# Optimization experiments

Measured on AMD Instinct MI355X. Metric: run time of the kernel, lower is better.

Reference implementation:

```python
import jax, jax.numpy as jnp
import numpy as np

NF, NC = 100000, 10000      # fact / company node counts
EF = 800000                 # edges per relation
DF, DC, H = 768, 128, 128   # fact dim, company dim, hidden
B = 256                     # graphs per batch


def setup_inputs() -> dict:
    key = jax.random.key(0)
    ks = jax.random.split(key, 24)
    s = 0.02
    inp = {
        "x_fact": jax.random.normal(ks[0], (NF, DF), jnp.float32),
        "x_company": jax.random.normal(ks[1], (NC, DC), jnp.float32),
        "ea_fc": jax.random.uniform(ks[2], (EF, 2), jnp.float32),
        "ea_cf": jax.random.uniform(ks[3], (EF, 2), jnp.float32),
        "fc_src": jax.random.randint(ks[4], (EF,), 0, NF),
        "fc_dst": jax.random.randint(ks[5], (EF,), 0, NC),
        "cf_src": jax.random.randint(ks[6], (EF,), 0, NC),
        "cf_dst": jax.random.randint(ks[7], (EF,), 0, NF),
        "batch_fact": jnp.sort(jax.random.randint(ks[8], (NF,), 0, B)),
        # edge gate Linear(2,1)
        "Wm": jax.random.normal(ks[9], (2, 1), jnp.float32) * s,
        "bm": jnp.zeros((1,), jnp.float32),
        # layer 1 GCNConv weights (lin applied to src features)
        "W1_fc": jax.random.normal(ks[10], (DF, H), jnp.float32) * s,
        "b1_fc": jnp.zeros((H,), jnp.float32),
        "W1_cf": jax.random.normal(ks[11], (DC, H), jnp.float32) * s,
        "b1_cf": jnp.zeros((H,), jnp.float32),
        # layer 2
        "W2_fc": jax.random.normal(ks[12], (H, H), jnp.float32) * s,
        "b2_fc": jnp.zeros((H,), jnp.float32),
        "W2_cf": jax.random.normal(ks[13], (H, H), jnp.float32) * s,
        "b2_cf": jnp.zeros((H,), jnp.float32),
        # classifier Linear(H, 1)
        "Wc": jax.random.normal(ks[14], (H, 1), jnp.float32) * s,
        "bc": jnp.zeros((1,), jnp.float32),
    }
    return inp


def _inv_sqrt(d):
    return jnp.where(d > 0, jax.lax.rsqrt(d), 0.0)


def _gcn(x_src, W, b, src, dst, w, n_src, n_dst):
    # symmetric-normalized weighted GCN conv (bipartite, no self loops)
    deg_s = jax.ops.segment_sum(w, src, num_segments=n_src)
    deg_d = jax.ops.segment_sum(w, dst, num_segments=n_dst)
    norm = w * _inv_sqrt(deg_s)[src] * _inv_sqrt(deg_d)[dst]  # [E]
    h = x_src @ W                                             # [n_src, H]
    out = jax.ops.segment_sum(norm[:, None] * h[src], dst, num_segments=n_dst)
    return out + b


def reference(x_fact, x_company, ea_fc, ea_cf, fc_src, fc_dst, cf_src, cf_dst,
              batch_fact, Wm, bm, W1_fc, b1_fc, W1_cf, b1_cf,
              W2_fc, b2_fc, W2_cf, b2_cf, Wc, bc):
    # learned per-edge gate: [sentiment, decay] -> sigmoid -> [0,1]
    w_fc = jax.nn.sigmoid(ea_fc @ Wm + bm)[:, 0]
    w_cf = jax.nn.sigmoid(ea_cf @ Wm + bm)[:, 0]

    # layer 1 (HeteroConv, aggr='sum'; one relation per dst type)
    c1 = jax.nn.relu(_gcn(x_fact, W1_fc, b1_fc, fc_src, fc_dst, w_fc, NF, NC))
    f1 = jax.nn.relu(_gcn(x_company, W1_cf, b1_cf, cf_src, cf_dst, w_cf, NC, NF))

    # layer 2
    c2 = jax.nn.relu(_gcn(f1, W2_fc, b2_fc, fc_src, fc_dst, w_fc, NF, NC))
    f2 = jax.nn.relu(_gcn(c1, W2_cf, b2_cf, cf_src, cf_dst, w_cf, NC, NF))

    # readout='fact': global mean pool over fact nodes per graph
    sums = jax.ops.segment_sum(f2, batch_fact, num_segments=B)        # [B, H]
    cnts = jax.ops.segment_sum(jnp.ones((NF,), f2.dtype), batch_fact, num_segments=B)
    pooled = sums / jnp.maximum(cnts, 1.0)[:, None]

    return (pooled @ Wc + bc)[:, 0]  # [B] logits
```

## Files before the change

kernel.cpp:

```cpp
#include <hip/hip_runtime.h>
#include <hip/hip_bf16.h>

#define NF 100000
#define NC 10000
#define EF 800000
#define DF 768
#define DC 128
#define H  128
#define B  256

#define GB1 782
#define GATEB 6250
#define SFC 192
#define SCF 32
#define MASK40 0xFFFFFFFFFFULL
#define FIXSCALE 1073741824.0f
#define INVFIX (1.0f/1073741824.0f)

typedef __bf16 bf16x8 __attribute__((ext_vector_type(8)));
typedef float  f32x4  __attribute__((ext_vector_type(4)));

#define GLD_LDS16(g, l) \
    __builtin_amdgcn_global_load_lds((const __attribute__((address_space(1))) void*)(g), \
                                     (__attribute__((address_space(3))) void*)(l), 16, 0, 0)

__global__ __launch_bounds__(256) void init_kernel(float4* __restrict__ zp, int nz4, int zb,
                                                   const float* __restrict__ W1,
                                                   __bf16* __restrict__ b1h,
                                                   __bf16* __restrict__ b1l) {
    if ((int)blockIdx.x < zb) {
        int i = blockIdx.x * 256 + threadIdx.x;
        if (i < nz4) zp[i] = make_float4(0.f, 0.f, 0.f, 0.f);
        return;
    }
    int idx = ((int)blockIdx.x - zb) * 256 + threadIdx.x;
    if (idx < DF * H) {
        int k = idx >> 7, n = idx & 127;
        float x = W1[idx];
        __bf16 h = (__bf16)x;
        b1h[n * DF + k] = h;
        b1l[n * DF + k] = (__bf16)(x - (float)h);
    }
}

__global__ __launch_bounds__(256) void gemm1_gate_kernel(
        const float* __restrict__ A,
        const __bf16* __restrict__ Bth, const __bf16* __restrict__ Btl,
        __bf16* __restrict__ Cb,
        const float* __restrict__ ea_fc, const float* __restrict__ ea_cf,
        const int* __restrict__ fc_src, const int* __restrict__ fc_dst,
        const int* __restrict__ cf_src, const int* __restrict__ cf_dst,
        const float* __restrict__ Wm, const float* __restrict__ bm,
        float* __restrict__ deg_s_fc, float* __restrict__ deg_s_cf,
        unsigned long long* __restrict__ packed_all,
        float2* __restrict__ pack_fc, float2* __restrict__ pack_cf) {
    __shared__ __attribute__((aligned(16))) __bf16 Bs[2][8192];
    const int K = DF, M = NF;
    int t = threadIdx.x;

    if ((int)blockIdx.x < GB1) {
        int lane = t & 63, wave = t >> 6;
        int row0 = blockIdx.x * 128;
        int m0 = wave * 32;
        int mrow = lane & 15;
        int kq = (lane >> 4) * 8;

        int soff[4];
        #pragma unroll
        for (int i = 0; i < 4; i++) {
            int s = wave * 256 + i * 64 + lane;
            int ks = s >> 9, nt = (s >> 6) & 7;
            int n  = nt * 16 + (lane & 15);
            int kk = ks * 32 + (lane >> 4) * 8;
            soff[i] = n * K + kk;
        }

        f32x4 acc[2][8] = {};

        for (int k0 = 0; k0 < K; k0 += 64) {
            __syncthreads();
            #pragma unroll
            for (int i = 0; i < 4; i++) {
                int base = (wave * 256 + i * 64) * 8;
                GLD_LDS16(Bth + soff[i] + k0, &Bs[0][base]);
                GLD_LDS16(Btl + soff[i] + k0, &Bs[1][base]);
            }
            bf16x8 ah[2][2], al[2][2];
            #pragma unroll
            for (int mt = 0; mt < 2; mt++) {
                int gr = row0 + m0 + mt * 16 + mrow;
                #pragma unroll
                for (int ks = 0; ks < 2; ks++) {
                    float f[8] = {0.f,0.f,0.f,0.f,0.f,0.f,0.f,0.f};
                    if (gr < M) {
                        const float* ap = &A[(size_t)gr * K + k0 + ks * 32 + kq];
                        float4 v0 = *(const float4*)ap;
                        float4 v1 = *(const float4*)(ap + 4);
                        f[0]=v0.x; f[1]=v0.y; f[2]=v0.z; f[3]=v0.w;
                        f[4]=v1.x; f[5]=v1.y; f[6]=v1.z; f[7]=v1.w;
                    }
                    #pragma unroll
                    for (int j = 0; j < 8; j++) {
                        __bf16 h = (__bf16)f[j];
                        ah[mt][ks][j] = h;
                        al[mt][ks][j] = (__bf16)(f[j] - (float)h);
                    }
                }
            }
            __syncthreads();
            #pragma unroll
            for (int ks = 0; ks < 2; ks++) {
                #pragma unroll
                for (int nt = 0; nt < 8; nt++) {
                    int slot = ks * 512 + nt * 64 + lane;
                    bf16x8 bh = *(const bf16x8*)&Bs[0][slot * 8];
                    bf16x8 bl = *(const bf16x8*)&Bs[1][slot * 8];
                    #pragma unroll
                    for (int mt = 0; mt < 2; mt++) {
                        acc[mt][nt] = __builtin_amdgcn_mfma_f32_16x16x32_bf16(ah[mt][ks], bh, acc[mt][nt], 0, 0, 0);
                        acc[mt][nt] = __builtin_amdgcn_mfma_f32_16x16x32_bf16(al[mt][ks], bh, acc[mt][nt], 0, 0, 0);
                        acc[mt][nt] = __builtin_amdgcn_mfma_f32_16x16x32_bf16(ah[mt][ks], bl, acc[mt][nt], 0, 0, 0);
                    }
                }
            }
        }
        #pragma unroll
        for (int mt = 0; mt < 2; mt++) {
            int gr0 = row0 + m0 + mt * 16 + (lane >> 4) * 4;
            #pragma unroll
            for (int nt = 0; nt < 8; nt++) {
                int col = nt * 16 + (lane & 15);
                #pragma unroll
                for (int r = 0; r < 4; r++) {
                    int gr = gr0 + r;
                    if (gr < M) Cb[(size_t)gr * 128 + col] = (__bf16)acc[mt][nt][r];
                }
            }
        }
    } else {
        int e = ((int)blockIdx.x - GB1) * 256 + t;
        bool is_cf = e >= EF;
        int ee = is_cf ? e - EF : e;
        const float2* ea = is_cf ? (const float2*)ea_cf : (const float2*)ea_fc;
        const int* src = is_cf ? cf_src : fc_src;
        const int* dst = is_cf ? cf_dst : fc_dst;
        float2 a = ea[ee];
        float z = a.x * Wm[0] + a.y * Wm[1] + bm[0];
        float w = 1.0f / (1.0f + expf(-z));
        int s = src[ee];
        int d = dst[ee];
        atomicAdd(is_cf ? &deg_s_cf[s] : &deg_s_fc[s], w);
        unsigned long long add = (1ULL << 40) | (unsigned long long)(w * FIXSCALE);
        unsigned long long old = atomicAdd(&packed_all[is_cf ? NC + d : d], add);
        int rank = (int)(old >> 40);
        if (is_cf) {
            if (rank < SCF) pack_cf[(size_t)d * SCF + rank] = make_float2(__int_as_float(s), w);
        } else {
            if (rank < SFC) pack_fc[(size_t)d * SFC + rank] = make_float2(__int_as_float(s), w);
        }
    }
}

__global__ __launch_bounds__(128) void agg_fc_w2_kernel(
        const float2* __restrict__ pack_fc,
        const unsigned long long* __restrict__ packed_fc,
        const float* __restrict__ deg_s_fc,
        const __bf16* __restrict__ h1b,
        const float* __restrict__ b1,
        const float* __restrict__ W2,
        __bf16* __restrict__ h2b) {
    int d = blockIdx.x;
    int t = threadIdx.x;
    unsigned long long pk = packed_fc[d];
    int cnt = (int)(pk >> 40); if (cnt > SFC) cnt = SFC;
    float dd = (float)(pk & MASK40) * INVFIX;
    float rdd = dd > 0.f ? rsqrtf(dd) : 0.f;
    __shared__ float2 s_e[SFC];
    __shared__ float c1row[H];
    const float2* bin = pack_fc + (size_t)d * SFC;
    for (int c = t; c < cnt; c += 128) {
        float2 p = bin[c];
        int s = __float_as_int(p.x);
        s_e[c] = make_float2(p.x, p.y * rsqrtf(deg_s_fc[s]));
    }
    __syncthreads();
    float acc = 0.f;
    #pragma unroll 8
    for (int j = 0; j < cnt; j++) {
        float2 p = s_e[j];
        acc += p.y * (float)h1b[(size_t)__float_as_int(p.x) * H + t];
    }
    float c1v = fmaxf(acc * rdd + b1[t], 0.f);
    c1row[t] = c1v;
    __syncthreads();
    float h2 = 0.f;
    #pragma unroll 8
    for (int k = 0; k < H; k++) h2 += c1row[k] * W2[k * H + t];
    h2b[(size_t)d * H + t] = (__bf16)h2;
}

#define FPB 8
__global__ __launch_bounds__(128) void agg_cf_pool_kernel(
        const float2* __restrict__ pack_cf,
        const unsigned long long* __restrict__ packed_cf,
        const float* __restrict__ deg_s_cf,
        const __bf16* __restrict__ h2b,
        const float* __restrict__ b2,
        const int* __restrict__ batch,
        float* __restrict__ pooled,
        float* __restrict__ bcnt) {
    int t = threadIdx.x;
    int f0 = blockIdx.x * FPB;
    __shared__ float2 s_e[FPB * SCF];
    __shared__ int   s_cnt[FPB];
    __shared__ int   s_batch[FPB];
    __shared__ float s_rdd[FPB];
    if (t < FPB) {
        unsigned long long pk = packed_cf[f0 + t];
        int cn = (int)(pk >> 40); if (cn > SCF) cn = SCF;
        s_cnt[t] = cn;
        float dd = (float)(pk & MASK40) * INVFIX;
        s_rdd[t] = dd > 0.f ? rsqrtf(dd) : 0.f;
        s_batch[t] = batch[f0 + t];
    }
    __syncthreads();
    #pragma unroll
    for (int c = 0; c < 2; c++) {
        int sl = c * 128 + t;
        int fl = sl >> 5, r = sl & 31;
        float2 v = make_float2(0.f, 0.f);
        if (r < s_cnt[fl]) {
            float2 p = pack_cf[(size_t)f0 * SCF + sl];
            int s = __float_as_int(p.x);
            v = make_float2(p.x, p.y * rsqrtf(deg_s_cf[s]));
        }
        s_e[sl] = v;
    }
    __syncthreads();
    float acc[FPB];
    #pragma unroll
    for (int f = 0; f < FPB; f++) {
        float a = 0.f;
        int cn = s_cnt[f];
        #pragma unroll 4
        for (int j = 0; j < cn; j++) {
            float2 p = s_e[f * SCF + j];
            a += p.y * (float)h2b[(size_t)__float_as_int(p.x) * H + t];
        }
        acc[f] = a;
    }
    float bval = b2[t];
    int cur_b = -1;
    float accp = 0.f;
    int runc = 0;
    #pragma unroll
    for (int f = 0; f < FPB; f++) {
        float val = fmaxf(acc[f] * s_rdd[f] + bval, 0.f);
        int b = s_batch[f];
        if (b != cur_b) {
            if (cur_b >= 0) {
                atomicAdd(&pooled[cur_b * H + t], accp);
                if (t == 0) atomicAdd(&bcnt[cur_b], (float)runc);
            }
            cur_b = b; accp = 0.f; runc = 0;
        }
        accp += val;
        runc++;
    }
    if (cur_b >= 0) {
        atomicAdd(&pooled[cur_b * H + t], accp);
        if (t == 0) atomicAdd(&bcnt[cur_b], (float)runc);
    }
}

__global__ void final_kernel(const float* __restrict__ pooled,
                             const float* __restrict__ bcnt,
                             const float* __restrict__ Wc,
                             const float* __restrict__ bc,
                             float* __restrict__ out) {
    int b = threadIdx.x;
    float sum = 0.f;
    #pragma unroll 8
    for (int k = 0; k < H; k++) sum += pooled[b * H + k] * Wc[k];
    float c = bcnt[b]; if (c < 1.f) c = 1.f;
    out[b] = sum / c + bc[0];
}

extern "C" void kernel_launch(void* const* d_in, const int* in_sizes, int n_in,
                              void* d_out, int out_size, void* d_ws, size_t ws_size,
                              hipStream_t stream) {
    const float* x_fact = (const float*)d_in[0];
    const float* ea_fc  = (const float*)d_in[2];
    const float* ea_cf  = (const float*)d_in[3];
    const int*   fc_src = (const int*)d_in[4];
    const int*   fc_dst = (const int*)d_in[5];
    const int*   cf_src = (const int*)d_in[6];
    const int*   cf_dst = (const int*)d_in[7];
    const int*   batch  = (const int*)d_in[8];
    const float* Wm     = (const float*)d_in[9];
    const float* bm     = (const float*)d_in[10];
    const float* W1_fc  = (const float*)d_in[11];
    const float* b1_fc  = (const float*)d_in[12];
    const float* W2_cf  = (const float*)d_in[17];
    const float* b2_cf  = (const float*)d_in[18];
    const float* Wc     = (const float*)d_in[19];
    const float* bc     = (const float*)d_in[20];
    float* out = (float*)d_out;

    char* wsb = (char*)d_ws;
    size_t o = 0;
    auto take = [&](size_t bytes) -> char* {
        char* p = wsb + o;
        o += (bytes + 255) & ~(size_t)255;
        return p;
    };

    const size_t PK_B  = ((size_t)(NC + NF) * 8 + 255) & ~(size_t)255;
    const size_t DSF_B = ((size_t)NF * 4 + 255) & ~(size_t)255;
    const size_t DSC_B = ((size_t)NC * 4 + 255) & ~(size_t)255;
    const size_t PL_B  = ((size_t)B * H * 4 + 255) & ~(size_t)255;
    const size_t BC_B  = ((size_t)B * 4 + 255) & ~(size_t)255;
    const size_t ZBYTES = PK_B + DSF_B + DSC_B + PL_B + BC_B;
    char* zbase = take(ZBYTES);
    unsigned long long* packed_all = (unsigned long long*)zbase;
    float* deg_s_fc = (float*)(zbase + PK_B);
    float* deg_s_cf = (float*)(zbase + PK_B + DSF_B);
    float* pooled   = (float*)(zbase + PK_B + DSF_B + DSC_B);
    float* bcnt     = (float*)(zbase + PK_B + DSF_B + DSC_B + PL_B);

    float2* pack_fc = (float2*)take((size_t)NC * SFC * 8);
    float2* pack_cf = (float2*)take((size_t)NF * SCF * 8);
    __bf16* h1b     = (__bf16*)take((size_t)NF * H * 2);
    __bf16* h2b     = (__bf16*)take((size_t)NC * H * 2);
    __bf16* b1h     = (__bf16*)take((size_t)DF * H * 2);
    __bf16* b1l     = (__bf16*)take((size_t)DF * H * 2);

    int nz4 = (int)(ZBYTES / 16);
    int zb = (nz4 + 255) / 256;
    int pb = (DF * H) / 256;
    init_kernel<<<zb + pb, 256, 0, stream>>>((float4*)zbase, nz4, zb, W1_fc, b1h, b1l);

    gemm1_gate_kernel<<<GB1 + GATEB, 256, 0, stream>>>(
        x_fact, b1h, b1l, h1b,
        ea_fc, ea_cf, fc_src, fc_dst, cf_src, cf_dst, Wm, bm,
        deg_s_fc, deg_s_cf, packed_all, pack_fc, pack_cf);

    agg_fc_w2_kernel<<<NC, 128, 0, stream>>>(pack_fc, packed_all, deg_s_fc,
                                             h1b, b1_fc, W2_cf, h2b);

    agg_cf_pool_kernel<<<NF / FPB, 128, 0, stream>>>(pack_cf, packed_all + NC,
                                                     deg_s_cf, h2b, b2_cf,
                                                     batch, pooled, bcnt);

    final_kernel<<<1, 256, 0, stream>>>(pooled, bcnt, Wc, bc, out);
}
```

Baseline: 741.0 us.

## Pad atomic counters, store fp32 features, vectorize gathers, batch gate edges per thread

Pads the per-node packed counters and degree accumulators to stride 8 or 16 elements so atomics on different nodes fall in separate cache lines. Stores h1 and h2 as fp32 instead of bf16 and gathers them with float4 loads, with four thread groups splitting edges and reducing through shared memory. The gate path handles four edges per thread with fewer blocks, and the pooling kernel processes 16 fact nodes per block. The padding greatly enlarges the zeroed region and fp32 features double the gather bytes, which may outweigh the reduced atomic contention.

```diff
diff --git a/kernel.cpp b/kernel.cpp
--- a/kernel.cpp
+++ b/kernel.cpp
@@ -10,9 +10,12 @@
 #define B  256
 
 #define GB1 782
-#define GATEB 6250
+#define GATEB 1563
 #define SFC 192
 #define SCF 32
+#define FPB 16
+#define PKS 8
+#define DSS 16
 #define MASK40 0xFFFFFFFFFFULL
 #define FIXSCALE 1073741824.0f
 #define INVFIX (1.0f/1073741824.0f)
@@ -46,7 +49,7 @@
 __global__ __launch_bounds__(256) void gemm1_gate_kernel(
         const float* __restrict__ A,
         const __bf16* __restrict__ Bth, const __bf16* __restrict__ Btl,
-        __bf16* __restrict__ Cb,
+        float* __restrict__ h1f,
         const float* __restrict__ ea_fc, const float* __restrict__ ea_cf,
         const int* __restrict__ fc_src, const int* __restrict__ fc_dst,
         const int* __restrict__ cf_src, const int* __restrict__ cf_dst,
@@ -133,129 +136,141 @@
                 #pragma unroll
                 for (int r = 0; r < 4; r++) {
                     int gr = gr0 + r;
-                    if (gr < M) Cb[(size_t)gr * 128 + col] = (__bf16)acc[mt][nt][r];
+                    if (gr < M) h1f[(size_t)gr * H + col] = acc[mt][nt][r];
                 }
             }
         }
     } else {
-        int e = ((int)blockIdx.x - GB1) * 256 + t;
-        bool is_cf = e >= EF;
-        int ee = is_cf ? e - EF : e;
-        const float2* ea = is_cf ? (const float2*)ea_cf : (const float2*)ea_fc;
-        const int* src = is_cf ? cf_src : fc_src;
-        const int* dst = is_cf ? cf_dst : fc_dst;
-        float2 a = ea[ee];
-        float z = a.x * Wm[0] + a.y * Wm[1] + bm[0];
-        float w = 1.0f / (1.0f + expf(-z));
-        int s = src[ee];
-        int d = dst[ee];
-        atomicAdd(is_cf ? &deg_s_cf[s] : &deg_s_fc[s], w);
-        unsigned long long add = (1ULL << 40) | (unsigned long long)(w * FIXSCALE);
-        unsigned long long old = atomicAdd(&packed_all[is_cf ? NC + d : d], add);
-        int rank = (int)(old >> 40);
-        if (is_cf) {
-            if (rank < SCF) pack_cf[(size_t)d * SCF + rank] = make_float2(__int_as_float(s), w);
-        } else {
-            if (rank < SFC) pack_fc[(size_t)d * SFC + rank] = make_float2(__int_as_float(s), w);
+        int ebase = ((int)blockIdx.x - GB1) * 1024 + t;
+        #pragma unroll
+        for (int i = 0; i < 4; i++) {
+            int e = ebase + i * 256;
+            if (e < 2 * EF) {
+                bool is_cf = e >= EF;
+                int ee = is_cf ? e - EF : e;
+                const float2* ea = is_cf ? (const float2*)ea_cf : (const float2*)ea_fc;
+                const int* srcp = is_cf ? cf_src : fc_src;
+                const int* dstp = is_cf ? cf_dst : fc_dst;
+                float2 a = ea[ee];
+                float z = a.x * Wm[0] + a.y * Wm[1] + bm[0];
+                float w = 1.0f / (1.0f + expf(-z));
+                int s = srcp[ee];
+                int d = dstp[ee];
+                atomicAdd(is_cf ? &deg_s_cf[(size_t)s * DSS] : &deg_s_fc[(size_t)s * DSS], w);
+                unsigned long long add = (1ULL << 40) | (unsigned long long)(w * FIXSCALE);
+                unsigned long long old = atomicAdd(&packed_all[(size_t)(is_cf ? NC + d : d) * PKS], add);
+                int rank = (int)(old >> 40);
+                if (is_cf) {
+                    if (rank < SCF) pack_cf[(size_t)d * SCF + rank] = make_float2(__int_as_float(s), w);
+                } else {
+                    if (rank < SFC) pack_fc[(size_t)d * SFC + rank] = make_float2(__int_as_float(s), w);
+                }
+            }
         }
     }
 }
 
 __global__ __launch_bounds__(128) void agg_fc_w2_kernel(
         const float2* __restrict__ pack_fc,
-        const unsigned long long* __restrict__ packed_fc,
+        const unsigned long long* __restrict__ packed_all,
         const float* __restrict__ deg_s_fc,
-        const __bf16* __restrict__ h1b,
+        const float* __restrict__ h1f,
         const float* __restrict__ b1,
         const float* __restrict__ W2,
-        __bf16* __restrict__ h2b) {
-    int d = blockIdx.x;
-    int t = threadIdx.x;
-    unsigned long long pk = packed_fc[d];
+        float* __restrict__ h2f) {
+    int d = blockIdx.x, t = threadIdx.x;
+    int g = t >> 5, c = t & 31;
+    unsigned long long pk = packed_all[(size_t)d * PKS];
     int cnt = (int)(pk >> 40); if (cnt > SFC) cnt = SFC;
     float dd = (float)(pk & MASK40) * INVFIX;
     float rdd = dd > 0.f ? rsqrtf(dd) : 0.f;
-    __shared__ float2 s_e[SFC];
+    __shared__ float2 s_rec[SFC];
+    __shared__ float red[4][H];
     __shared__ float c1row[H];
     const float2* bin = pack_fc + (size_t)d * SFC;
-    for (int c = t; c < cnt; c += 128) {
-        float2 p = bin[c];
+    for (int j = t; j < cnt; j += 128) {
+        float2 p = bin[j];
         int s = __float_as_int(p.x);
-        s_e[c] = make_float2(p.x, p.y * rsqrtf(deg_s_fc[s]));
-    }
-    __syncthreads();
-    float acc = 0.f;
-    #pragma unroll 8
-    for (int j = 0; j < cnt; j++) {
-        float2 p = s_e[j];
-        acc += p.y * (float)h1b[(size_t)__float_as_int(p.x) * H + t];
-    }
-    float c1v = fmaxf(acc * rdd + b1[t], 0.f);
-    c1row[t] = c1v;
+        s_rec[j] = make_float2(p.x, p.y * rsqrtf(deg_s_fc[(size_t)s * DSS]));
+    }
+    __syncthreads();
+    float ax = 0.f, ay = 0.f, az = 0.f, aw = 0.f;
+    #pragma unroll 4
+    for (int j = g; j < cnt; j += 4) {
+        float2 p = s_rec[j];
+        const float4 v = *(const float4*)&h1f[(size_t)__float_as_int(p.x) * H + c * 4];
+        ax += p.y * v.x; ay += p.y * v.y; az += p.y * v.z; aw += p.y * v.w;
+    }
+    red[g][c*4+0] = ax; red[g][c*4+1] = ay; red[g][c*4+2] = az; red[g][c*4+3] = aw;
+    __syncthreads();
+    float a = red[0][t] + red[1][t] + red[2][t] + red[3][t];
+    c1row[t] = fmaxf(a * rdd + b1[t], 0.f);
     __syncthreads();
     float h2 = 0.f;
     #pragma unroll 8
     for (int k = 0; k < H; k++) h2 += c1row[k] * W2[k * H + t];
-    h2b[(size_t)d * H + t] = (__bf16)h2;
-}
-
-#define FPB 8
+    h2f[(size_t)d * H + t] = h2;
+}
+
 __global__ __launch_bounds__(128) void agg_cf_pool_kernel(
         const float2* __restrict__ pack_cf,
-        const unsigned long long* __restrict__ packed_cf,
+        const unsigned long long* __restrict__ packed_all,
         const float* __restrict__ deg_s_cf,
-        const __bf16* __restrict__ h2b,
+        const float* __restrict__ h2f,
         const float* __restrict__ b2,
         const int* __restrict__ batch,
         float* __restrict__ pooled,
         float* __restrict__ bcnt) {
-    int t = threadIdx.x;
-    int f0 = blockIdx.x * FPB;
-    __shared__ float2 s_e[FPB * SCF];
-    __shared__ int   s_cnt[FPB];
-    __shared__ int   s_batch[FPB];
+    int t = threadIdx.x, f0 = blockIdx.x * FPB;
+    int g = t >> 5, c = t & 31;
+    __shared__ float2 s_rec[FPB * SCF];
+    __shared__ float f2buf[FPB][H];
+    __shared__ int   s_cnt[FPB], s_batch[FPB];
     __shared__ float s_rdd[FPB];
     if (t < FPB) {
-        unsigned long long pk = packed_cf[f0 + t];
+        unsigned long long pk = packed_all[(size_t)(NC + f0 + t) * PKS];
         int cn = (int)(pk >> 40); if (cn > SCF) cn = SCF;
         s_cnt[t] = cn;
-        float dd = (float)(pk & MASK40) * INVFIX;
-        s_rdd[t] = dd > 0.f ? rsqrtf(dd) : 0.f;
+        float ddv = (float)(pk & MASK40) * INVFIX;
+        s_rdd[t] = ddv > 0.f ? rsqrtf(ddv) : 0.f;
         s_batch[t] = batch[f0 + t];
     }
     __syncthreads();
     #pragma unroll
-    for (int c = 0; c < 2; c++) {
-        int sl = c * 128 + t;
-        int fl = sl >> 5, r = sl & 31;
+    for (int i = 0; i < 4; i++) {
+        int sl = i * 128 + t, fl = sl >> 5, r = sl & 31;
         float2 v = make_float2(0.f, 0.f);
         if (r < s_cnt[fl]) {
-            float2 p = pack_cf[(size_t)f0 * SCF + sl];
-            int s = __float_as_int(p.x);
-            v = make_float2(p.x, p.y * rsqrtf(deg_s_cf[s]));
-        }
-        s_e[sl] = v;
-    }
-    __syncthreads();
-    float acc[FPB];
+            float2 p = pack_cf[(size_t)(f0 + fl) * SCF + r];
+            v = make_float2(p.x, p.y * rsqrtf(deg_s_cf[(size_t)__float_as_int(p.x) * DSS]));
+        }
+        s_rec[sl] = v;
+    }
+    __syncthreads();
     #pragma unroll
-    for (int f = 0; f < FPB; f++) {
-        float a = 0.f;
+    for (int fi = 0; fi < 4; fi++) {
+        int f = g + fi * 4;
         int cn = s_cnt[f];
+        float ax = 0.f, ay = 0.f, az = 0.f, aw = 0.f;
         #pragma unroll 4
         for (int j = 0; j < cn; j++) {
-            float2 p = s_e[f * SCF + j];
-            a += p.y * (float)h2b[(size_t)__float_as_int(p.x) * H + t];
-        }
-        acc[f] = a;
-    }
-    float bval = b2[t];
+            float2 p = s_rec[f * SCF + j];
+            const float4 v = *(const float4*)&h2f[(size_t)__float_as_int(p.x) * H + c * 4];
+            ax += p.y * v.x; ay += p.y * v.y; az += p.y * v.z; aw += p.y * v.w;
+        }
+        float rddv = s_rdd[f];
+        f2buf[f][c*4+0] = fmaxf(ax * rddv + b2[c*4+0], 0.f);
+        f2buf[f][c*4+1] = fmaxf(ay * rddv + b2[c*4+1], 0.f);
+        f2buf[f][c*4+2] = fmaxf(az * rddv + b2[c*4+2], 0.f);
+        f2buf[f][c*4+3] = fmaxf(aw * rddv + b2[c*4+3], 0.f);
+    }
+    __syncthreads();
     int cur_b = -1;
     float accp = 0.f;
     int runc = 0;
     #pragma unroll
     for (int f = 0; f < FPB; f++) {
-        float val = fmaxf(acc[f] * s_rdd[f] + bval, 0.f);
+        float val = f2buf[f][t];
         int b = s_batch[f];
         if (b != cur_b) {
             if (cur_b >= 0) {
@@ -315,9 +330,9 @@
         return p;
     };
 
-    const size_t PK_B  = ((size_t)(NC + NF) * 8 + 255) & ~(size_t)255;
-    const size_t DSF_B = ((size_t)NF * 4 + 255) & ~(size_t)255;
-    const size_t DSC_B = ((size_t)NC * 4 + 255) & ~(size_t)255;
+    const size_t PK_B  = ((size_t)(NC + NF) * PKS * 8 + 255) & ~(size_t)255;
+    const size_t DSF_B = ((size_t)NF * DSS * 4 + 255) & ~(size_t)255;
+    const size_t DSC_B = ((size_t)NC * DSS * 4 + 255) & ~(size_t)255;
     const size_t PL_B  = ((size_t)B * H * 4 + 255) & ~(size_t)255;
     const size_t BC_B  = ((size_t)B * 4 + 255) & ~(size_t)255;
     const size_t ZBYTES = PK_B + DSF_B + DSC_B + PL_B + BC_B;
@@ -330,8 +345,8 @@
 
     float2* pack_fc = (float2*)take((size_t)NC * SFC * 8);
     float2* pack_cf = (float2*)take((size_t)NF * SCF * 8);
-    __bf16* h1b     = (__bf16*)take((size_t)NF * H * 2);
-    __bf16* h2b     = (__bf16*)take((size_t)NC * H * 2);
+    float*  h1f     = (float*)take((size_t)NF * H * 4);
+    float*  h2f     = (float*)take((size_t)NC * H * 4);
     __bf16* b1h     = (__bf16*)take((size_t)DF * H * 2);
     __bf16* b1l     = (__bf16*)take((size_t)DF * H * 2);
 
@@ -341,15 +356,15 @@
     init_kernel<<<zb + pb, 256, 0, stream>>>((float4*)zbase, nz4, zb, W1_fc, b1h, b1l);
 
     gemm1_gate_kernel<<<GB1 + GATEB, 256, 0, stream>>>(
-        x_fact, b1h, b1l, h1b,
+        x_fact, b1h, b1l, h1f,
         ea_fc, ea_cf, fc_src, fc_dst, cf_src, cf_dst, Wm, bm,
         deg_s_fc, deg_s_cf, packed_all, pack_fc, pack_cf);
 
     agg_fc_w2_kernel<<<NC, 128, 0, stream>>>(pack_fc, packed_all, deg_s_fc,
-                                             h1b, b1_fc, W2_cf, h2b);
-
-    agg_cf_pool_kernel<<<NF / FPB, 128, 0, stream>>>(pack_cf, packed_all + NC,
-                                                     deg_s_cf, h2b, b2_cf,
+                                             h1f, b1_fc, W2_cf, h2f);
+
+    agg_cf_pool_kernel<<<NF / FPB, 128, 0, stream>>>(pack_cf, packed_all,
+                                                     deg_s_cf, h2f, b2_cf,
                                                      batch, pooled, bcnt);
 
     final_kernel<<<1, 256, 0, stream>>>(pooled, bcnt, Wc, bc, out);
```

Result: no change. 738.3 us (-0.4%).
